# Kernel tuning notes

Measured on AMD Instinct MI355X. Metric: run time of the kernel, lower is better.

## Reference

```python
import jax, jax.numpy as jnp
import numpy as np

IN_DIM = 64
OUT_DIM = 128
GROUPS = 4
KS = 3
PAD = 1
SPLINE_ORDER = 3
GRID_SIZE = 5
GRID_K = GRID_SIZE + SPLINE_ORDER  # 8
GRID_LO, GRID_HI = -1.0, 1.0
_H = (GRID_HI - GRID_LO) / GRID_SIZE
GRID = jnp.linspace(GRID_LO - _H * SPLINE_ORDER, GRID_HI + _H * SPLINE_ORDER,
                    GRID_SIZE + 2 * SPLINE_ORDER + 1, dtype=jnp.float32)  # [14]
EPS = 1e-5


def _conv(x, w):
    # NCHW x OIHW -> NCHW, stride 1, dilation 1, padding PAD
    return jax.lax.conv_general_dilated(
        x, w, window_strides=(1, 1), padding=((PAD, PAD), (PAD, PAD)),
        dimension_numbers=('NCHW', 'OIHW', 'NCHW'))


def _bspline_bases(x):
    # Cox-de-Boor recursion; x: [B,C,H,W] -> [B, C*GRID_K, H, W]
    xu = x[..., None]  # [B,C,H,W,1]
    g = GRID
    bases = ((xu >= g[:-1]) & (xu < g[1:])).astype(x.dtype)  # [B,C,H,W,13]
    for k in range(1, SPLINE_ORDER + 1):
        left = g[:-(k + 1)]
        right = g[k:-1]
        delta = jnp.where(right == left, jnp.ones_like(right), right - left)
        bases = ((xu - left) / delta * bases[..., :-1]
                 + (g[k + 1:] - xu) / (g[k + 1:] - g[1:-k]) * bases[..., 1:])
    B, C, H, W, K = bases.shape  # K == GRID_K
    # moveaxis(-1, 2) then flatten(1, 2): channel-major, basis-minor ordering
    return jnp.moveaxis(bases, -1, 2).reshape(B, C * K, H, W)


def setup_inputs() -> dict:
    key = jax.random.key(0)
    k1, k2 = jax.random.split(key)
    x = jax.random.normal(k1, (8, IN_DIM, 64, 64), dtype=jnp.float32)
    # layer_weight: [out/g, (in/g)*(grid_k+1), ks, ks] = [32, 144, 3, 3]
    layer_weight = jax.random.normal(
        k2, (OUT_DIM // GROUPS, (IN_DIM // GROUPS) * (GRID_K + 1), KS, KS),
        dtype=jnp.float32) * 0.05
    prelu_w = jnp.full((GROUPS,), 0.25, dtype=jnp.float32)  # torch PReLU init
    return {"x": x, "layer_weight": layer_weight, "prelu_w": prelu_w}


def reference(x, layer_weight, prelu_w):
    cin_g = IN_DIM // GROUPS
    cout_g = OUT_DIM // GROUPS
    base_w = layer_weight[:, -cin_g:].reshape(cout_g, cin_g, KS, KS)
    spline_w = layer_weight[:, :-cin_g].reshape(cout_g, cin_g * GRID_K, KS, KS)
    outs = []
    for g in range(GROUPS):
        xg = x[:, g * cin_g:(g + 1) * cin_g]
        base_out = _conv(jax.nn.gelu(xg, approximate=False), base_w)
        spline_out = _conv(_bspline_bases(xg), spline_w)
        y = base_out + spline_out
        # InstanceNorm2d (affine=False): per-sample per-channel spatial norm
        mu = y.mean(axis=(2, 3), keepdims=True)
        var = y.var(axis=(2, 3), keepdims=True)
        y = (y - mu) / jnp.sqrt(var + EPS)
        # PReLU with scalar slope per group
        y = jnp.where(y >= 0, y, prelu_w[g] * y)
        outs.append(y)
    return jnp.concatenate(outs, axis=1)  # [B, OUT_DIM, H, W]
```

## Files before the change

kernel.cpp:

```cpp
#include <hip/hip_runtime.h>
#include <hip/hip_bf16.h>
#include <math.h>

typedef __attribute__((ext_vector_type(8))) short short8;
typedef __attribute__((ext_vector_type(4))) float f32x4;
typedef __attribute__((ext_vector_type(16))) float f32x16;
typedef unsigned int u32;
typedef unsigned long long u64;

__device__ __forceinline__ ushort f2bf(float f) {
    u32 u = __float_as_uint(f);
    return (ushort)((u + 0x7fffu + ((u >> 16) & 1u)) >> 16);
}
__device__ __forceinline__ float bf2f(ushort h) {
    return __uint_as_float(((u32)h) << 16);
}
__device__ __forceinline__ u32 cvtpk_bf16(float a, float b) {
    u32 r;
    asm("v_cvt_pk_bf16_f32 %0, %1, %2" : "=v"(r) : "v"(a), "v"(b));
    return r;
}

__global__ void wtrans(const float* __restrict__ lw, ushort* __restrict__ w2) {
    int t = blockIdx.x * 256 + threadIdx.x;
    if (t >= 5184) return;
    int l    = t & 63;
    int page = t >> 6;
    int ks  = page % 9;
    int tap = page / 9;
    int oc = l & 31;
    int kbase = ks * 16 + ((l >> 5) << 3);
    short8 v;
#pragma unroll
    for (int e = 0; e < 8; ++e) {
        int k = kbase + e;
        v[e] = (short)f2bf(lw[(oc * 144 + k) * 9 + tap]);
    }
    ((short8*)w2)[t] = v;
}

__global__ __launch_bounds__(256, 4) void kanconv(const float* __restrict__ x,
                                                  const ushort* __restrict__ w2,
                                                  ushort* __restrict__ yraw) {
    __shared__ __align__(16) ushort Fs[109 * 152];
    const int tid  = threadIdx.x;
    const int tile = blockIdx.x;
    const int b    = blockIdx.y;
    const int g    = blockIdx.z;
    const int h0 = (tile >> 2) * 4;
    const int w0 = (tile & 3) * 16;
    const float* xg = x + ((size_t)(b * 64 + g * 16)) * 4096;

    float xv1[4], xv2[4];
    unsigned imgbits = 0;
#pragma unroll
    for (int it = 0; it < 4; ++it) {
        int e = it * 256 + tid;
        int icg = e / 108;
        int p   = e - icg * 108;
        int py = p / 18, px = p - py * 18;
        int hy = h0 + py - 1, wx = w0 + px - 1;
        bool valid = (e < 864) && ((unsigned)hy < 64u) && ((unsigned)wx < 64u);
        int off = valid ? (icg * 4096 + hy * 64 + wx) : 0;
        float a = xg[off];
        float c = xg[off + 8 * 4096];
        if (!valid) { a = 0.f; c = 0.f; } else { imgbits |= (1u << it); }
        xv1[it] = a;
        xv2[it] = c;
    }

#define STAGE(V, IMGF, ROWP, SLOT)                                            \
    do {                                                                      \
        float v_ = (V);                                                       \
        float tpos_ = (v_ + 2.2f) * 2.5f;                                     \
        float cf_ = floorf(tpos_);                                            \
        int ci_ = (int)cf_;                                                   \
        float u_ = tpos_ - cf_;                                               \
        float u2_ = u_ * u_, u3_ = u2_ * u_, om_ = 1.f - u_;                  \
        float q0_ = om_ * om_ * om_ * (1.f / 6.f);                            \
        float q1_ = (4.f - 6.f * u2_ + 3.f * u3_) * (1.f / 6.f);              \
        float q2_ = (1.f + 3.f * u_ + 3.f * u2_ - 3.f * u3_) * (1.f / 6.f);   \
        float q3_ = u3_ * (1.f / 6.f);                                        \
        u64 Q_ = (u64)cvtpk_bf16(q0_, q1_)                                    \
               | ((u64)cvtpk_bf16(q2_, q3_) << 32);                           \
        u64 lo_ = 0, hi_ = 0;                                                 \
        if ((IMGF) && ci_ >= 0 && ci_ <= 10) {                                \
            int s_ = ci_ * 16 - 48;                                           \
            if (s_ < 0)       { lo_ = Q_ >> (-s_); }                          \
            else if (s_ < 64) { lo_ = Q_ << s_;                               \
                                hi_ = s_ ? (Q_ >> (64 - s_)) : 0ull; }        \
            else              { hi_ = Q_ << (s_ - 64); }                      \
        }                                                                     \
        union { u64 q[2]; short8 s8; } un_;                                   \
        un_.q[0] = lo_; un_.q[1] = hi_;                                       \
        ushort* row_ = &Fs[(ROWP) * 152];                                     \
        *(short8*)(row_ + (SLOT) * 8) = un_.s8;                               \
        float x3_ = v_ * v_ * v_;                                             \
        float t2_ = fmaf(0.0713548163f, x3_, 1.5957691216f * v_);             \
        float e2_ = __expf(t2_);                                              \
        float th_ = 1.f - 2.f / (e2_ + 1.f);                                  \
        float ge_ = 0.5f * v_ * (1.f + th_);                                  \
        row_[128 + (SLOT)] = f2bf(ge_);                                       \
    } while (0)

#define STAGE_IT(IT, XV, SB)                                                  \
    do {                                                                      \
        int e_ = (IT) * 256 + tid;                                            \
        int icg_ = e_ / 108;                                                  \
        int p_ = e_ - icg_ * 108;                                             \
        int rowp_ = (e_ < 864) ? p_ : 108;         \
        bool im_ = (imgbits >> (IT)) & 1u;                                    \
        STAGE((XV)[IT], im_, rowp_, icg_ + (SB));                             \
    } while (0)

    STAGE_IT(0, xv1, 0);
    STAGE_IT(1, xv1, 0);
    STAGE_IT(2, xv1, 0);
    STAGE_IT(3, xv1, 0);
    __syncthreads();

    const int wv = tid >> 6;
    const int l  = tid & 63;
    const int la = l & 31, klo = l >> 5;
    const int p0row = la >> 4, p0col = la & 15;
    const short8* w8 = (const short8*)w2;

    f32x16 accA, accB;
#pragma unroll
    for (int i = 0; i < 16; ++i) { accA[i] = 0.f; accB[i] = 0.f; }

#define TAPKS(TAP, K0, K1)                                                     \
    do {                                                                       \
        const int kh_ = (TAP) / 3, kw_ = (TAP) - kh_ * 3;                      \
        const ushort* fb0_ =                                                   \
            &Fs[((p0row + kh_) * 18 + (p0col + kw_)) * 152 + klo * 8];         \
        const ushort* fb1_ = fb0_ + 2 * 18 * 152;                              \
        const short8* ap_ = w8 + (TAP) * 576 + l;                              \
        _Pragma("unroll")                                                      \
        for (int ks_ = (K0); ks_ < (K1); ++ks_) {                              \
            short8 a_  = ap_[ks_ * 64];                                        \
            short8 b0_ = *(const short8*)(fb0_ + ks_ * 16);                    \
            short8 b1_ = *(const short8*)(fb1_ + ks_ * 16);                    \
            accA = __builtin_amdgcn_mfma_f32_32x32x16_bf16(a_, b0_, accA, 0, 0, 0); \
            accB = __builtin_amdgcn_mfma_f32_32x32x16_bf16(a_, b1_, accB, 0, 0, 0); \
        }                                                                      \
    } while (0)

    const int t0 = wv * 2, t1 = wv * 2 + 1;

    STAGE_IT(0, xv2, 8);
    STAGE_IT(1, xv2, 8);
    TAPKS(t0, 0, 2);
    STAGE_IT(2, xv2, 8);
    TAPKS(t0, 2, 4);
    STAGE_IT(3, xv2, 8);
    TAPKS(t1, 0, 4);
    if (wv == 3) TAPKS(8, 0, 4);
    __syncthreads();

    TAPKS(t0, 4, 9);
    TAPKS(t1, 4, 9);
    if (wv == 3) TAPKS(8, 4, 9);
#undef TAPKS
#undef STAGE_IT
#undef STAGE

    __syncthreads();
    float* comb = (float*)Fs;
    if (wv != 0) {
        float* cp = comb + ((wv - 1) * 64 + l) * 20;
        *(f32x4*)(cp + 0)  = f32x4{accA[0], accA[1], accA[2], accA[3]};
        *(f32x4*)(cp + 4)  = f32x4{accA[4], accA[5], accA[6], accA[7]};
        *(f32x4*)(cp + 8)  = f32x4{accA[8], accA[9], accA[10], accA[11]};
        *(f32x4*)(cp + 12) = f32x4{accA[12], accA[13], accA[14], accA[15]};
    }
    if (wv != 1) {
        int slot = (wv == 0) ? 3 : (2 + wv);
        float* cp = comb + (slot * 64 + l) * 20;
        *(f32x4*)(cp + 0)  = f32x4{accB[0], accB[1], accB[2], accB[3]};
        *(f32x4*)(cp + 4)  = f32x4{accB[4], accB[5], accB[6], accB[7]};
        *(f32x4*)(cp + 8)  = f32x4{accB[8], accB[9], accB[10], accB[11]};
        *(f32x4*)(cp + 12) = f32x4{accB[12], accB[13], accB[14], accB[15]};
    }
    __syncthreads();
    if (wv < 2) {
        f32x16 sum = (wv == 0) ? accA : accB;
        const int sbase = (wv == 0) ? 0 : 3;
#pragma unroll
        for (int s = 0; s < 3; ++s) {
            const float* cp = comb + ((sbase + s) * 64 + l) * 20;
            f32x4 c0 = *(const f32x4*)(cp + 0);
            f32x4 c1 = *(const f32x4*)(cp + 4);
            f32x4 c2 = *(const f32x4*)(cp + 8);
            f32x4 c3 = *(const f32x4*)(cp + 12);
#pragma unroll
            for (int r = 0; r < 4; ++r) {
                sum[r]      += c0[r];
                sum[r + 4]  += c1[r];
                sum[r + 8]  += c2[r];
                sum[r + 12] += c3[r];
            }
        }
        const int pix = wv * 32 + la;
        const int prow = pix >> 4, pcol = pix & 15;
        ushort* yb = yraw + (((size_t)b * 128 + g * 32) * 64 + h0 + prow) * 64
                          + w0 + pcol;
#pragma unroll
        for (int r = 0; r < 16; ++r) {
            int oc = (r & 3) + 8 * (r >> 2) + 4 * klo;
            yb[(size_t)oc * 4096] = f2bf(sum[r]);
        }
    }
}

__global__ __launch_bounds__(256) void instnorm(const ushort* __restrict__ yraw,
                                                float* __restrict__ y,
                                                const float* __restrict__ prelu) {
    const int blk = blockIdx.x;
    const int tid = threadIdx.x;
    const short8* rp = (const short8*)(yraw + (size_t)blk * 4096);
    short8 a = rp[tid * 2], c = rp[tid * 2 + 1];
    float v[16];
#pragma unroll
    for (int j = 0; j < 8; ++j) {
        v[j]     = bf2f((ushort)a[j]);
        v[8 + j] = bf2f((ushort)c[j]);
    }
    float s = 0.f, s2 = 0.f;
#pragma unroll
    for (int j = 0; j < 16; ++j) { s += v[j]; s2 += v[j] * v[j]; }
#pragma unroll
    for (int off = 32; off > 0; off >>= 1) {
        s  += __shfl_down(s, off);
        s2 += __shfl_down(s2, off);
    }
    __shared__ float red[8];
    int wave = tid >> 6;
    if ((tid & 63) == 0) { red[wave] = s; red[4 + wave] = s2; }
    __syncthreads();
    float S  = red[0] + red[1] + red[2] + red[3];
    float S2 = red[4] + red[5] + red[6] + red[7];
    float mean = S * (1.0f / 4096.0f);
    float var  = S2 * (1.0f / 4096.0f) - mean * mean;
    float rstd = rsqrtf(var + 1e-5f);
    float slope = prelu[(blk >> 5) & 3];
    float4* op = (float4*)(y + (size_t)blk * 4096) + tid * 4;
#pragma unroll
    for (int k = 0; k < 4; ++k) {
        float4 o;
        float t;
        t = (v[k * 4 + 0] - mean) * rstd; o.x = t >= 0.f ? t : slope * t;
        t = (v[k * 4 + 1] - mean) * rstd; o.y = t >= 0.f ? t : slope * t;
        t = (v[k * 4 + 2] - mean) * rstd; o.z = t >= 0.f ? t : slope * t;
        t = (v[k * 4 + 3] - mean) * rstd; o.w = t >= 0.f ? t : slope * t;
        op[k] = o;
    }
}

extern "C" void kernel_launch(void* const* d_in, const int* in_sizes, int n_in,
                              void* d_out, int out_size, void* d_ws, size_t ws_size,
                              hipStream_t stream) {
    const float* x     = (const float*)d_in[0];
    const float* lw    = (const float*)d_in[1];
    const float* prelu = (const float*)d_in[2];
    float*  out  = (float*)d_out;
    ushort* w2   = (ushort*)d_ws;
    ushort* yraw = (ushort*)((char*)d_ws + 92160);

    wtrans<<<21, 256, 0, stream>>>(lw, w2);
    dim3 grid(64, 8, 4);
    kanconv<<<grid, 256, 0, stream>>>(x, w2, yraw);
    instnorm<<<1024, 256, 0, stream>>>(yraw, out, prelu);
}
```

Before: 39.87 us.

## Fuse instance norm into conv kernel via grid-wide barrier and partial stats

The separate instnorm kernel is removed and its work folded into the conv kernel. Each block now does two tiles and writes per-tile, per-channel sum and sum-of-squares partials to a workspace buffer. All blocks then wait on a spin barrier driven by an atomic counter, reduce the partials, and normalize and apply PReLU to the tiles they produced. This saves a kernel launch and the full-tensor statistics pass. The cost is that all 1024 blocks must be co-resident, otherwise the barrier deadlocks until the spin cap is hit, and blocks sit idle while waiting at the barrier.

```diff
diff --git a/kernel.cpp b/kernel.cpp
--- a/kernel.cpp
+++ b/kernel.cpp
@@ -21,7 +21,12 @@
     return r;
 }
 
-__global__ void wtrans(const float* __restrict__ lw, ushort* __restrict__ w2) {
+#define PARTS_SQ 131072
+
+__global__ void wtrans(const float* __restrict__ lw, ushort* __restrict__ w2,
+                       u32* __restrict__ cnt) {
+    if (blockIdx.x == 0 && threadIdx.x == 0)
+        __hip_atomic_store(cnt, 0u, __ATOMIC_RELAXED, __HIP_MEMORY_SCOPE_AGENT);
     int t = blockIdx.x * 256 + threadIdx.x;
     if (t >= 5184) return;
     int l    = t & 63;
@@ -41,33 +46,26 @@
 
 __global__ __launch_bounds__(256, 4) void kanconv(const float* __restrict__ x,
                                                   const ushort* __restrict__ w2,
-                                                  ushort* __restrict__ yraw) {
+                                                  ushort* __restrict__ yraw,
+                                                  float* __restrict__ parts,
+                                                  u32* __restrict__ cnt,
+                                                  float* __restrict__ out,
+                                                  const float* __restrict__ prelu) {
     __shared__ __align__(16) ushort Fs[109 * 152];
     const int tid  = threadIdx.x;
-    const int tile = blockIdx.x;
-    const int b    = blockIdx.y;
-    const int g    = blockIdx.z;
-    const int h0 = (tile >> 2) * 4;
-    const int w0 = (tile & 3) * 16;
+    const int beta = blockIdx.x;
+    const int bg   = beta >> 5;
+    const int lt2  = beta & 31;
+    const int b = bg >> 2, g = bg & 3;
+    const int m = lt2 & 7;
+    const int q = lt2 >> 3;
     const float* xg = x + ((size_t)(b * 64 + g * 16)) * 4096;
 
-    float xv1[4], xv2[4];
-    unsigned imgbits = 0;
-#pragma unroll
-    for (int it = 0; it < 4; ++it) {
-        int e = it * 256 + tid;
-        int icg = e / 108;
-        int p   = e - icg * 108;
-        int py = p / 18, px = p - py * 18;
-        int hy = h0 + py - 1, wx = w0 + px - 1;
-        bool valid = (e < 864) && ((unsigned)hy < 64u) && ((unsigned)wx < 64u);
-        int off = valid ? (icg * 4096 + hy * 64 + wx) : 0;
-        float a = xg[off];
-        float c = xg[off + 8 * 4096];
-        if (!valid) { a = 0.f; c = 0.f; } else { imgbits |= (1u << it); }
-        xv1[it] = a;
-        xv2[it] = c;
-    }
+    const int wv = tid >> 6;
+    const int l  = tid & 63;
+    const int la = l & 31, klo = l >> 5;
+    const int p0row = la >> 4, p0col = la & 15;
+    const short8* w8 = (const short8*)w2;
 
 #define STAGE(V, IMGF, ROWP, SLOT)                                            \
     do {                                                                      \
@@ -91,8 +89,8 @@
                                 hi_ = s_ ? (Q_ >> (64 - s_)) : 0ull; }        \
             else              { hi_ = Q_ << (s_ - 64); }                      \
         }                                                                     \
-        union { u64 q[2]; short8 s8; } un_;                                   \
-        un_.q[0] = lo_; un_.q[1] = hi_;                                       \
+        union { u64 qq[2]; short8 s8; } un_;                                  \
+        un_.qq[0] = lo_; un_.qq[1] = hi_;                                     \
         ushort* row_ = &Fs[(ROWP) * 152];                                     \
         *(short8*)(row_ + (SLOT) * 8) = un_.s8;                               \
         float x3_ = v_ * v_ * v_;                                             \
@@ -112,22 +110,6 @@
         bool im_ = (imgbits >> (IT)) & 1u;                                    \
         STAGE((XV)[IT], im_, rowp_, icg_ + (SB));                             \
     } while (0)
-
-    STAGE_IT(0, xv1, 0);
-    STAGE_IT(1, xv1, 0);
-    STAGE_IT(2, xv1, 0);
-    STAGE_IT(3, xv1, 0);
-    __syncthreads();
-
-    const int wv = tid >> 6;
-    const int l  = tid & 63;
-    const int la = l & 31, klo = l >> 5;
-    const int p0row = la >> 4, p0col = la & 15;
-    const short8* w8 = (const short8*)w2;
-
-    f32x16 accA, accB;
-#pragma unroll
-    for (int i = 0; i < 16; ++i) { accA[i] = 0.f; accB[i] = 0.f; }
 
 #define TAPKS(TAP, K0, K1)                                                     \
     do {                                                                       \
@@ -146,114 +128,194 @@
         }                                                                      \
     } while (0)
 
-    const int t0 = wv * 2, t1 = wv * 2 + 1;
-
-    STAGE_IT(0, xv2, 8);
-    STAGE_IT(1, xv2, 8);
-    TAPKS(t0, 0, 2);
-    STAGE_IT(2, xv2, 8);
-    TAPKS(t0, 2, 4);
-    STAGE_IT(3, xv2, 8);
-    TAPKS(t1, 0, 4);
-    if (wv == 3) TAPKS(8, 0, 4);
-    __syncthreads();
-
-    TAPKS(t0, 4, 9);
-    TAPKS(t1, 4, 9);
-    if (wv == 3) TAPKS(8, 4, 9);
+#pragma unroll 1
+    for (int pass = 0; pass < 2; ++pass) {
+        const int tile = m * 8 + q + pass * 4;
+        const int h0 = (2 * m + pass) * 4;
+        const int w0 = q * 16;
+
+        float xv1[4], xv2[4];
+        unsigned imgbits = 0;
+#pragma unroll
+        for (int it = 0; it < 4; ++it) {
+            int e = it * 256 + tid;
+            int icg = e / 108;
+            int p   = e - icg * 108;
+            int py = p / 18, px = p - py * 18;
+            int hy = h0 + py - 1, wx = w0 + px - 1;
+            bool valid = (e < 864) && ((unsigned)hy < 64u) && ((unsigned)wx < 64u);
+            int off = valid ? (icg * 4096 + hy * 64 + wx) : 0;
+            float a = xg[off];
+            float c = xg[off + 8 * 4096];
+            if (!valid) { a = 0.f; c = 0.f; } else { imgbits |= (1u << it); }
+            xv1[it] = a;
+            xv2[it] = c;
+        }
+
+        STAGE_IT(0, xv1, 0);
+        STAGE_IT(1, xv1, 0);
+        STAGE_IT(2, xv1, 0);
+        STAGE_IT(3, xv1, 0);
+        __syncthreads();
+
+        f32x16 accA, accB;
+#pragma unroll
+        for (int i = 0; i < 16; ++i) { accA[i] = 0.f; accB[i] = 0.f; }
+        const int t0 = wv * 2, t1 = wv * 2 + 1;
+
+        STAGE_IT(0, xv2, 8);
+        STAGE_IT(1, xv2, 8);
+        TAPKS(t0, 0, 2);
+        STAGE_IT(2, xv2, 8);
+        TAPKS(t0, 2, 4);
+        STAGE_IT(3, xv2, 8);
+        TAPKS(t1, 0, 4);
+        if (wv == 3) TAPKS(8, 0, 4);
+        __syncthreads();
+
+        TAPKS(t0, 4, 9);
+        TAPKS(t1, 4, 9);
+        if (wv == 3) TAPKS(8, 4, 9);
+
+        __syncthreads();
+        float* comb = (float*)Fs;
+        if (wv != 0) {
+            float* cp = comb + ((wv - 1) * 64 + l) * 20;
+            *(f32x4*)(cp + 0)  = f32x4{accA[0], accA[1], accA[2], accA[3]};
+            *(f32x4*)(cp + 4)  = f32x4{accA[4], accA[5], accA[6], accA[7]};
+            *(f32x4*)(cp + 8)  = f32x4{accA[8], accA[9], accA[10], accA[11]};
+            *(f32x4*)(cp + 12) = f32x4{accA[12], accA[13], accA[14], accA[15]};
+        }
+        if (wv != 1) {
+            int slot = (wv == 0) ? 3 : (2 + wv);
+            float* cp = comb + (slot * 64 + l) * 20;
+            *(f32x4*)(cp + 0)  = f32x4{accB[0], accB[1], accB[2], accB[3]};
+            *(f32x4*)(cp + 4)  = f32x4{accB[4], accB[5], accB[6], accB[7]};
+            *(f32x4*)(cp + 8)  = f32x4{accB[8], accB[9], accB[10], accB[11]};
+            *(f32x4*)(cp + 12) = f32x4{accB[12], accB[13], accB[14], accB[15]};
+        }
+        __syncthreads();
+        if (wv < 2) {
+            f32x16 sum = (wv == 0) ? accA : accB;
+            const int sbase = (wv == 0) ? 0 : 3;
+#pragma unroll
+            for (int s = 0; s < 3; ++s) {
+                const float* cp = comb + ((sbase + s) * 64 + l) * 20;
+                f32x4 c0 = *(const f32x4*)(cp + 0);
+                f32x4 c1 = *(const f32x4*)(cp + 4);
+                f32x4 c2 = *(const f32x4*)(cp + 8);
+                f32x4 c3 = *(const f32x4*)(cp + 12);
+#pragma unroll
+                for (int r = 0; r < 4; ++r) {
+                    sum[r]      += c0[r];
+                    sum[r + 4]  += c1[r];
+                    sum[r + 8]  += c2[r];
+                    sum[r + 12] += c3[r];
+                }
+            }
+            const int pix = wv * 32 + la;
+            const int prow = pix >> 4, pcol = pix & 15;
+            ushort* yb = yraw + (((size_t)b * 128 + g * 32) * 64 + h0 + prow) * 64
+                              + w0 + pcol;
+#pragma unroll
+            for (int r = 0; r < 16; ++r) {
+                int oc = (r & 3) + 8 * (r >> 2) + 4 * klo;
+                yb[(size_t)oc * 4096] = f2bf(sum[r]);
+            }
+            float s_[16], q_[16];
+#pragma unroll
+            for (int r = 0; r < 16; ++r) { s_[r] = sum[r]; q_[r] = sum[r] * sum[r]; }
+#pragma unroll
+            for (int off = 16; off >= 1; off >>= 1) {
+#pragma unroll
+                for (int r = 0; r < 16; ++r) {
+                    s_[r] += __shfl_xor(s_[r], off);
+                    q_[r] += __shfl_xor(q_[r], off);
+                }
+            }
+            if (la == 0) {
+                size_t sb = ((size_t)(bg * 2 + klo) * 16) * 128 + tile * 2 + wv;
+#pragma unroll
+                for (int r = 0; r < 16; ++r) {
+                    __hip_atomic_store(&parts[sb + (size_t)r * 128], s_[r],
+                                       __ATOMIC_RELAXED, __HIP_MEMORY_SCOPE_AGENT);
+                    __hip_atomic_store(&parts[PARTS_SQ + sb + (size_t)r * 128], q_[r],
+                                       __ATOMIC_RELAXED, __HIP_MEMORY_SCOPE_AGENT);
+                }
+            }
+        }
+        __syncthreads();
+    }
 #undef TAPKS
 #undef STAGE_IT
 #undef STAGE
 
+    if (tid == 0) {
+        __hip_atomic_fetch_add(cnt, 1u, __ATOMIC_ACQ_REL, __HIP_MEMORY_SCOPE_AGENT);
+        int spins = 0;
+        while (__hip_atomic_load(cnt, __ATOMIC_ACQUIRE,
+                                 __HIP_MEMORY_SCOPE_AGENT) < 1024u) {
+            if (++spins > 3000000) break;
+            __builtin_amdgcn_s_sleep(1);
+        }
+    }
     __syncthreads();
-    float* comb = (float*)Fs;
-    if (wv != 0) {
-        float* cp = comb + ((wv - 1) * 64 + l) * 20;
-        *(f32x4*)(cp + 0)  = f32x4{accA[0], accA[1], accA[2], accA[3]};
-        *(f32x4*)(cp + 4)  = f32x4{accA[4], accA[5], accA[6], accA[7]};
-        *(f32x4*)(cp + 8)  = f32x4{accA[8], accA[9], accA[10], accA[11]};
-        *(f32x4*)(cp + 12) = f32x4{accA[12], accA[13], accA[14], accA[15]};
-    }
-    if (wv != 1) {
-        int slot = (wv == 0) ? 3 : (2 + wv);
-        float* cp = comb + (slot * 64 + l) * 20;
-        *(f32x4*)(cp + 0)  = f32x4{accB[0], accB[1], accB[2], accB[3]};
-        *(f32x4*)(cp + 4)  = f32x4{accB[4], accB[5], accB[6], accB[7]};
-        *(f32x4*)(cp + 8)  = f32x4{accB[8], accB[9], accB[10], accB[11]};
-        *(f32x4*)(cp + 12) = f32x4{accB[12], accB[13], accB[14], accB[15]};
+
+    float* fscr = (float*)Fs;
+    {
+        int j = tid >> 3, seg = tid & 7;
+        int klo2 = j >> 4, r2 = j & 15;
+        size_t base = ((size_t)(bg * 2 + klo2) * 16 + r2) * 128;
+        float ss = 0.f, sq = 0.f;
+#pragma unroll
+        for (int s = 0; s < 16; ++s) {
+            int idx = seg * 16 + s;
+            ss += __hip_atomic_load(&parts[base + idx], __ATOMIC_RELAXED,
+                                    __HIP_MEMORY_SCOPE_AGENT);
+            sq += __hip_atomic_load(&parts[PARTS_SQ + base + idx], __ATOMIC_RELAXED,
+                                    __HIP_MEMORY_SCOPE_AGENT);
+        }
+        fscr[j * 8 + seg]       = ss;
+        fscr[256 + j * 8 + seg] = sq;
     }
     __syncthreads();
-    if (wv < 2) {
-        f32x16 sum = (wv == 0) ? accA : accB;
-        const int sbase = (wv == 0) ? 0 : 3;
-#pragma unroll
-        for (int s = 0; s < 3; ++s) {
-            const float* cp = comb + ((sbase + s) * 64 + l) * 20;
-            f32x4 c0 = *(const f32x4*)(cp + 0);
-            f32x4 c1 = *(const f32x4*)(cp + 4);
-            f32x4 c2 = *(const f32x4*)(cp + 8);
-            f32x4 c3 = *(const f32x4*)(cp + 12);
-#pragma unroll
-            for (int r = 0; r < 4; ++r) {
-                sum[r]      += c0[r];
-                sum[r + 4]  += c1[r];
-                sum[r + 8]  += c2[r];
-                sum[r + 12] += c3[r];
-            }
-        }
-        const int pix = wv * 32 + la;
-        const int prow = pix >> 4, pcol = pix & 15;
-        ushort* yb = yraw + (((size_t)b * 128 + g * 32) * 64 + h0 + prow) * 64
-                          + w0 + pcol;
-#pragma unroll
-        for (int r = 0; r < 16; ++r) {
-            int oc = (r & 3) + 8 * (r >> 2) + 4 * klo;
-            yb[(size_t)oc * 4096] = f2bf(sum[r]);
-        }
-    }
-}
-
-__global__ __launch_bounds__(256) void instnorm(const ushort* __restrict__ yraw,
-                                                float* __restrict__ y,
-                                                const float* __restrict__ prelu) {
-    const int blk = blockIdx.x;
-    const int tid = threadIdx.x;
-    const short8* rp = (const short8*)(yraw + (size_t)blk * 4096);
-    short8 a = rp[tid * 2], c = rp[tid * 2 + 1];
-    float v[16];
-#pragma unroll
-    for (int j = 0; j < 8; ++j) {
-        v[j]     = bf2f((ushort)a[j]);
-        v[8 + j] = bf2f((ushort)c[j]);
-    }
-    float s = 0.f, s2 = 0.f;
-#pragma unroll
-    for (int j = 0; j < 16; ++j) { s += v[j]; s2 += v[j] * v[j]; }
-#pragma unroll
-    for (int off = 32; off > 0; off >>= 1) {
-        s  += __shfl_down(s, off);
-        s2 += __shfl_down(s2, off);
-    }
-    __shared__ float red[8];
-    int wave = tid >> 6;
-    if ((tid & 63) == 0) { red[wave] = s; red[4 + wave] = s2; }
+    if (tid < 32) {
+        float S = 0.f, S2 = 0.f;
+#pragma unroll
+        for (int s = 0; s < 8; ++s) { S += fscr[tid * 8 + s]; S2 += fscr[256 + tid * 8 + s]; }
+        int klo2 = tid >> 4, r2 = tid & 15;
+        int oc = (r2 & 3) + 8 * (r2 >> 2) + 4 * klo2;
+        float mean = S * (1.0f / 4096.0f);
+        float var  = S2 * (1.0f / 4096.0f) - mean * mean;
+        fscr[512 + oc] = mean;
+        fscr[544 + oc] = rsqrtf(var + 1e-5f);
+    }
     __syncthreads();
-    float S  = red[0] + red[1] + red[2] + red[3];
-    float S2 = red[4] + red[5] + red[6] + red[7];
-    float mean = S * (1.0f / 4096.0f);
-    float var  = S2 * (1.0f / 4096.0f) - mean * mean;
-    float rstd = rsqrtf(var + 1e-5f);
-    float slope = prelu[(blk >> 5) & 3];
-    float4* op = (float4*)(y + (size_t)blk * 4096) + tid * 4;
-#pragma unroll
-    for (int k = 0; k < 4; ++k) {
-        float4 o;
-        float t;
-        t = (v[k * 4 + 0] - mean) * rstd; o.x = t >= 0.f ? t : slope * t;
-        t = (v[k * 4 + 1] - mean) * rstd; o.y = t >= 0.f ? t : slope * t;
-        t = (v[k * 4 + 2] - mean) * rstd; o.z = t >= 0.f ? t : slope * t;
-        t = (v[k * 4 + 3] - mean) * rstd; o.w = t >= 0.f ? t : slope * t;
-        op[k] = o;
+    {
+        const float slope = prelu[g];
+        int seg = tid >> 1, half = tid & 1;
+        int oc = seg >> 2, r = seg & 3;
+        float mean = fscr[512 + oc];
+        float rstd = fscr[544 + oc];
+#pragma unroll
+        for (int pass = 0; pass < 2; ++pass) {
+            int h0 = (2 * m + pass) * 4, w0 = q * 16;
+            size_t idx = (((size_t)(b * 128 + g * 32 + oc)) * 64 + h0 + r) * 64
+                       + w0 + half * 8;
+            short8 yv = *(const short8*)(yraw + idx);
+            float4 o0, o1;
+            float t;
+            t = (bf2f((ushort)yv[0]) - mean) * rstd; o0.x = t >= 0.f ? t : slope * t;
+            t = (bf2f((ushort)yv[1]) - mean) * rstd; o0.y = t >= 0.f ? t : slope * t;
+            t = (bf2f((ushort)yv[2]) - mean) * rstd; o0.z = t >= 0.f ? t : slope * t;
+            t = (bf2f((ushort)yv[3]) - mean) * rstd; o0.w = t >= 0.f ? t : slope * t;
+            t = (bf2f((ushort)yv[4]) - mean) * rstd; o1.x = t >= 0.f ? t : slope * t;
+            t = (bf2f((ushort)yv[5]) - mean) * rstd; o1.y = t >= 0.f ? t : slope * t;
+            t = (bf2f((ushort)yv[6]) - mean) * rstd; o1.z = t >= 0.f ? t : slope * t;
+            t = (bf2f((ushort)yv[7]) - mean) * rstd; o1.w = t >= 0.f ? t : slope * t;
+            *(float4*)(out + idx)     = o0;
+            *(float4*)(out + idx + 4) = o1;
+        }
     }
 }
 
@@ -263,12 +325,12 @@
     const float* x     = (const float*)d_in[0];
     const float* lw    = (const float*)d_in[1];
     const float* prelu = (const float*)d_in[2];
-    float*  out  = (float*)d_out;
-    ushort* w2   = (ushort*)d_ws;
-    ushort* yraw = (ushort*)((char*)d_ws + 92160);
-
-    wtrans<<<21, 256, 0, stream>>>(lw, w2);
-    dim3 grid(64, 8, 4);
-    kanconv<<<grid, 256, 0, stream>>>(x, w2, yraw);
-    instnorm<<<1024, 256, 0, stream>>>(yraw, out, prelu);
-}
+    float*  out   = (float*)d_out;
+    ushort* w2    = (ushort*)d_ws;
+    ushort* yraw  = (ushort*)((char*)d_ws + 131072);
+    float*  parts = (float*)((char*)d_ws + 131072 + 8388608);
+    u32*    cnt   = (u32*)((char*)d_ws + 131072 + 8388608 + 1048576);
+
+    wtrans<<<21, 256, 0, stream>>>(lw, w2, cnt);
+    kanconv<<<1024, 256, 0, stream>>>(x, w2, yraw, parts, cnt, out, prelu);
+}
```

New measurement: 142.5 us. 3.57x slower.
